# Kernel optimization log

Measured on AMD Instinct MI355X. Metric: run time of the kernel, lower is better.

Reference implementation:

```python
import jax, jax.numpy as jnp
import numpy as np

NUM_RBF = 16
NUM_POS_EMBED = 16
D_MIN, D_MAX = 0.0, 20.0
N_NODES = 20000
N_EDGES = 640000


def _ideal_virtual_cb(bb):
    # bb: [N, 4, 3] with atoms (N, CA, C, O)
    N, CA, C = bb[:, 0], bb[:, 1], bb[:, 2]
    b = CA - N
    c = C - CA
    a = jnp.cross(b, c)
    return -0.58273431 * a + 0.56802827 * b - 0.54067466 * c + CA


def _rbf(D, D_min, D_max, D_count):
    # D: [..., 1] -> [..., D_count]
    D_mu = jnp.linspace(D_min, D_max, D_count, dtype=D.dtype)
    D_sigma = (D_max - D_min) / D_count
    return jnp.exp(-(((D - D_mu) / D_sigma) ** 2))


def _edge_positional_embeddings(edge_index, num_embeddings):
    d = (edge_index[0] - edge_index[1]).astype(jnp.float32)  # [E]
    freq = jnp.exp(
        jnp.arange(0, num_embeddings, 2, dtype=jnp.float32)
        * -(np.log(10000.0) / num_embeddings)
    )  # [num_embeddings//2]
    angles = d[:, None] * freq  # [E, num_embeddings//2]
    return jnp.concatenate([jnp.cos(angles), jnp.sin(angles)], axis=-1)


def setup_inputs() -> dict:
    key = jax.random.key(0)
    k1, k2 = jax.random.split(key)
    bb = jax.random.normal(k1, (N_NODES, 4, 3), dtype=jnp.float32)
    edge_index = jax.random.randint(k2, (2, N_EDGES), 0, N_NODES, dtype=jnp.int64)
    return {"bb": bb, "edge_index": edge_index}


def reference(bb, edge_index, eps=1e-8):
    dst = edge_index[0]
    src = edge_index[1]
    num_edges = edge_index.shape[-1]

    virtual_cb = _ideal_virtual_cb(bb)                     # [N, 3]
    bb5 = jnp.concatenate([bb, virtual_cb[:, None, :]], axis=-2)  # [N, 5, 3]

    edge_bb_src = bb5[src]                                 # [E, 5, 3]
    edge_bb_dst = bb5[dst]                                 # [E, 5, 3]
    diff = edge_bb_src[:, :, None, :] - edge_bb_dst[:, None, :, :] + eps  # [E,5,5,3]
    dists = jnp.linalg.norm(diff, axis=-1)                 # [E, 5, 5]
    dists = dists.reshape(num_edges, -1, 1)                # [E, 25, 1]

    edge_rbf = _rbf(dists, D_MIN, D_MAX, NUM_RBF)          # [E, 25, 16]
    edge_rbf = edge_rbf.reshape(num_edges, -1)             # [E, 400]

    pos = _edge_positional_embeddings(edge_index, NUM_POS_EMBED)  # [E, 16]

    return jnp.concatenate([edge_rbf, pos], axis=-1).astype(jnp.float32)  # [E, 416]
```

## Files before the change

### kernel.cpp

```cpp
#include <hip/hip_runtime.h>
#include <hip/hip_bf16.h>

#define NN 20000
#define NE 640000
#define FEAT 416
#define EPB 16
#define EDGE_BLOCKS (NE / EPB)

typedef float f32x4 __attribute__((ext_vector_type(4)));


__global__ __launch_bounds__(256) void prep_kernel(const float* __restrict__ bb,
                                                   const int* __restrict__ ei,
                                                   int* __restrict__ flag,
                                                   float* __restrict__ bb5) {
    int t = blockIdx.x * 256 + threadIdx.x;

    if (blockIdx.x == 0 && threadIdx.x < 64) {
        int v = ei[2 * threadIdx.x + 1];
        unsigned long long m = __ballot(v != 0);
        if (threadIdx.x == 0) flag[0] = (m == 0ULL) ? 2 : 1;
    }

    if (t < NN) {
        const float* r = bb + (size_t)t * 12;
        float Nx = r[0], Ny = r[1], Nz = r[2];
        float CAx = r[3], CAy = r[4], CAz = r[5];
        float Cx = r[6], Cy = r[7], Cz = r[8];
        float Ox = r[9], Oy = r[10], Oz = r[11];
        float bx = CAx - Nx, by = CAy - Ny, bz = CAz - Nz;
        float cx = Cx - CAx, cy = Cy - CAy, cz = Cz - CAz;
        float ax = by * cz - bz * cy;
        float ay = bz * cx - bx * cz;
        float az = bx * cy - by * cx;
        float vx = -0.58273431f * ax + 0.56802827f * bx - 0.54067466f * cx + CAx;
        float vy = -0.58273431f * ay + 0.56802827f * by - 0.54067466f * cy + CAy;
        float vz = -0.58273431f * az + 0.56802827f * bz - 0.54067466f * cz + CAz;
        float* w = bb5 + (size_t)t * 15;
        w[0] = Nx;  w[1] = Ny;  w[2] = Nz;
        w[3] = CAx; w[4] = CAy; w[5] = CAz;
        w[6] = Cx;  w[7] = Cy;  w[8] = Cz;
        w[9] = Ox;  w[10] = Oy; w[11] = Oz;
        w[12] = vx; w[13] = vy; w[14] = vz;
    }
}

__device__ __forceinline__ void load_idx(const int* __restrict__ ei, int sel, int e,
                                         int& dst, int& src) {
    if (sel == 2) {
        dst = ei[2 * e];
        src = ei[2 * (NE + e)];
    } else {
        dst = ei[e];
        src = ei[NE + e];
    }
}

__global__ __launch_bounds__(256) void edge_kernel(const int* __restrict__ ei,
                                                   const float* __restrict__ bb5,
                                                   const int* __restrict__ flag,
                                                   float* __restrict__ out) {
    __shared__ float dist[EPB * 25];
    __shared__ int sidx[EPB * 2];

    const int tid = threadIdx.x;
    const int e0 = blockIdx.x * EPB;

    if (tid < EPB) {
        int dst, src;
        load_idx(ei, flag[0], e0 + tid, dst, src);
        sidx[tid * 2] = dst;
        sidx[tid * 2 + 1] = src;
    }
    __syncthreads();

    for (int item = tid; item < EPB * 25; item += 256) {
        int s = item / 25;
        int p = item - s * 25;
        int i = p / 5;
        int j = p - i * 5;
        int dst = sidx[s * 2], src = sidx[s * 2 + 1];
        const float* S = bb5 + src * 15 + i * 3;
        const float* D = bb5 + dst * 15 + j * 3;
        float dx = S[0] - D[0] + 1e-8f;
        float dy = S[1] - D[1] + 1e-8f;
        float dz = S[2] - D[2] + 1e-8f;
        dist[item] = sqrtf(dx * dx + dy * dy + dz * dz) * 0.8f;
    }

    f32x4* out4 = reinterpret_cast<f32x4*>(out) + (size_t)e0 * 104;

    if (tid < EPB * 4) {
        int s = tid >> 2;
        int g = tid & 3;
        int dst = sidx[s * 2], src = sidx[s * 2 + 1];
        float d = (float)(dst - src);
        int fb = (g & 1) * 4;
        bool issin = (g >= 2);
        float v[4];
#pragma unroll
        for (int k = 0; k < 4; ++k) {
            int f = fb + k;
            float freq = expf(-(float)f * (float)(9.210340371976184 / 8.0));
            float angle = d * freq;
            double t = (double)angle * 0.15915494309189535;
            double r = t - rint(t);
            float rf = (float)r;
            float val;
            if (issin) {
                asm("v_sin_f32 %0, %1" : "=v"(val) : "v"(rf));
            } else {
                asm("v_cos_f32 %0, %1" : "=v"(val) : "v"(rf));
            }
            v[k] = val;
        }
        f32x4 r4;
        r4.x = v[0]; r4.y = v[1]; r4.z = v[2]; r4.w = v[3];
        __builtin_nontemporal_store(r4, &out4[s * 104 + 100 + g]);
    }
    __syncthreads();

    for (int item = tid; item < EPB * 100; item += 256) {
        int s = item / 100;
        int c = item - s * 100;
        int p = c >> 2;
        int g = c & 3;
        float a = dist[s * 25 + p];
        int k0 = g * 4;
        f32x4 r;
        float u;
        u = a - (float)(k0 + 0) * (16.0f / 15.0f); r.x = __expf(-(u * u));
        u = a - (float)(k0 + 1) * (16.0f / 15.0f); r.y = __expf(-(u * u));
        u = a - (float)(k0 + 2) * (16.0f / 15.0f); r.z = __expf(-(u * u));
        u = a - (float)(k0 + 3) * (16.0f / 15.0f); r.w = __expf(-(u * u));
        __builtin_nontemporal_store(r, &out4[s * 104 + c]);
    }
}

extern "C" void kernel_launch(void* const* d_in, const int* in_sizes, int n_in,
                              void* d_out, int out_size, void* d_ws, size_t ws_size,
                              hipStream_t stream) {
    const float* bb = (const float*)d_in[0];
    const int* ei = (const int*)d_in[1];
    int* flag = (int*)d_ws;
    float* bb5 = (float*)((char*)d_ws + 64);
    float* out = (float*)d_out;

    hipLaunchKernelGGL(prep_kernel, dim3((NN + 255) / 256), dim3(256), 0, stream,
                       bb, ei, flag, bb5);
    hipLaunchKernelGGL(edge_kernel, dim3(EDGE_BLOCKS), dim3(256), 0, stream,
                       ei, bb5, flag, out);
}
```

Before: 228.1 us.

## Fuse virtual-CB prep into edge kernel and drop nontemporal stores

Removes the separate prep kernel and its bb5 workspace. Each edge block now loads the raw backbone rows for its 32 endpoint nodes, computes the virtual CB in registers and stages the 5x3 coordinates in shared memory. Every block redoes the index-format ballot check itself. The aim is to save one launch and the global write and read of bb5, at the cost of recomputing the virtual CB per edge endpoint. Output stores also change from nontemporal to ordinary stores, which alters the cache behaviour for the large output stream.

```diff
diff --git a/kernel.cpp b/kernel.cpp
--- a/kernel.cpp
+++ b/kernel.cpp
@@ -8,42 +8,6 @@
 #define EDGE_BLOCKS (NE / EPB)
 
 typedef float f32x4 __attribute__((ext_vector_type(4)));
-
-
-__global__ __launch_bounds__(256) void prep_kernel(const float* __restrict__ bb,
-                                                   const int* __restrict__ ei,
-                                                   int* __restrict__ flag,
-                                                   float* __restrict__ bb5) {
-    int t = blockIdx.x * 256 + threadIdx.x;
-
-    if (blockIdx.x == 0 && threadIdx.x < 64) {
-        int v = ei[2 * threadIdx.x + 1];
-        unsigned long long m = __ballot(v != 0);
-        if (threadIdx.x == 0) flag[0] = (m == 0ULL) ? 2 : 1;
-    }
-
-    if (t < NN) {
-        const float* r = bb + (size_t)t * 12;
-        float Nx = r[0], Ny = r[1], Nz = r[2];
-        float CAx = r[3], CAy = r[4], CAz = r[5];
-        float Cx = r[6], Cy = r[7], Cz = r[8];
-        float Ox = r[9], Oy = r[10], Oz = r[11];
-        float bx = CAx - Nx, by = CAy - Ny, bz = CAz - Nz;
-        float cx = Cx - CAx, cy = Cy - CAy, cz = Cz - CAz;
-        float ax = by * cz - bz * cy;
-        float ay = bz * cx - bx * cz;
-        float az = bx * cy - by * cx;
-        float vx = -0.58273431f * ax + 0.56802827f * bx - 0.54067466f * cx + CAx;
-        float vy = -0.58273431f * ay + 0.56802827f * by - 0.54067466f * cy + CAy;
-        float vz = -0.58273431f * az + 0.56802827f * bz - 0.54067466f * cz + CAz;
-        float* w = bb5 + (size_t)t * 15;
-        w[0] = Nx;  w[1] = Ny;  w[2] = Nz;
-        w[3] = CAx; w[4] = CAy; w[5] = CAz;
-        w[6] = Cx;  w[7] = Cy;  w[8] = Cz;
-        w[9] = Ox;  w[10] = Oy; w[11] = Oz;
-        w[12] = vx; w[13] = vy; w[14] = vz;
-    }
-}
 
 __device__ __forceinline__ void load_idx(const int* __restrict__ ei, int sel, int e,
                                          int& dst, int& src) {
@@ -56,21 +20,48 @@
     }
 }
 
-__global__ __launch_bounds__(256) void edge_kernel(const int* __restrict__ ei,
-                                                   const float* __restrict__ bb5,
-                                                   const int* __restrict__ flag,
-                                                   float* __restrict__ out) {
+__global__ __launch_bounds__(256) void fused_kernel(const float* __restrict__ bb,
+                                                    const int* __restrict__ ei,
+                                                    float* __restrict__ out) {
+    __shared__ float rows[2 * EPB][17];
     __shared__ float dist[EPB * 25];
     __shared__ int sidx[EPB * 2];
 
     const int tid = threadIdx.x;
     const int e0 = blockIdx.x * EPB;
 
-    if (tid < EPB) {
-        int dst, src;
-        load_idx(ei, flag[0], e0 + tid, dst, src);
-        sidx[tid * 2] = dst;
-        sidx[tid * 2 + 1] = src;
+    if (tid < 64) {
+        int pv = ei[2 * tid + 1];
+        unsigned long long m = __ballot(pv != 0);
+        int sel = (m == 0ULL) ? 2 : 1;
+
+        if (tid < 2 * EPB) {
+            int e = e0 + (tid >> 1);
+            int dst, src;
+            load_idx(ei, sel, e, dst, src);
+            int node = (tid & 1) ? src : dst;
+            sidx[tid] = node;
+            const f32x4* bv = (const f32x4*)bb + (size_t)node * 3;
+            f32x4 v0 = bv[0], v1 = bv[1], v2 = bv[2];
+            float Nx = v0.x, Ny = v0.y, Nz = v0.z;
+            float CAx = v0.w, CAy = v1.x, CAz = v1.y;
+            float Cx = v1.z, Cy = v1.w, Cz = v2.x;
+            float Ox = v2.y, Oy = v2.z, Oz = v2.w;
+            float bx = CAx - Nx, by = CAy - Ny, bz = CAz - Nz;
+            float cx = Cx - CAx, cy = Cy - CAy, cz = Cz - CAz;
+            float ax = by * cz - bz * cy;
+            float ay = bz * cx - bx * cz;
+            float az = bx * cy - by * cx;
+            float vx = -0.58273431f * ax + 0.56802827f * bx - 0.54067466f * cx + CAx;
+            float vy = -0.58273431f * ay + 0.56802827f * by - 0.54067466f * cy + CAy;
+            float vz = -0.58273431f * az + 0.56802827f * bz - 0.54067466f * cz + CAz;
+            float* w = rows[tid];
+            w[0] = Nx;  w[1] = Ny;  w[2] = Nz;
+            w[3] = CAx; w[4] = CAy; w[5] = CAz;
+            w[6] = Cx;  w[7] = Cy;  w[8] = Cz;
+            w[9] = Ox;  w[10] = Oy; w[11] = Oz;
+            w[12] = vx; w[13] = vy; w[14] = vz;
+        }
     }
     __syncthreads();
 
@@ -79,9 +70,8 @@
         int p = item - s * 25;
         int i = p / 5;
         int j = p - i * 5;
-        int dst = sidx[s * 2], src = sidx[s * 2 + 1];
-        const float* S = bb5 + src * 15 + i * 3;
-        const float* D = bb5 + dst * 15 + j * 3;
+        const float* S = rows[2 * s + 1] + i * 3;
+        const float* D = rows[2 * s] + j * 3;
         float dx = S[0] - D[0] + 1e-8f;
         float dy = S[1] - D[1] + 1e-8f;
         float dz = S[2] - D[2] + 1e-8f;
@@ -116,7 +106,7 @@
         }
         f32x4 r4;
         r4.x = v[0]; r4.y = v[1]; r4.z = v[2]; r4.w = v[3];
-        __builtin_nontemporal_store(r4, &out4[s * 104 + 100 + g]);
+        out4[s * 104 + 100 + g] = r4;
     }
     __syncthreads();
 
@@ -133,7 +123,7 @@
         u = a - (float)(k0 + 1) * (16.0f / 15.0f); r.y = __expf(-(u * u));
         u = a - (float)(k0 + 2) * (16.0f / 15.0f); r.z = __expf(-(u * u));
         u = a - (float)(k0 + 3) * (16.0f / 15.0f); r.w = __expf(-(u * u));
-        __builtin_nontemporal_store(r, &out4[s * 104 + c]);
+        out4[s * 104 + c] = r;
     }
 }
 
@@ -142,12 +132,8 @@
                               hipStream_t stream) {
     const float* bb = (const float*)d_in[0];
     const int* ei = (const int*)d_in[1];
-    int* flag = (int*)d_ws;
-    float* bb5 = (float*)((char*)d_ws + 64);
     float* out = (float*)d_out;
 
-    hipLaunchKernelGGL(prep_kernel, dim3((NN + 255) / 256), dim3(256), 0, stream,
-                       bb, ei, flag, bb5);
-    hipLaunchKernelGGL(edge_kernel, dim3(EDGE_BLOCKS), dim3(256), 0, stream,
-                       ei, bb5, flag, out);
+    hipLaunchKernelGGL(fused_kernel, dim3(EDGE_BLOCKS), dim3(256), 0, stream,
+                       bb, ei, out);
 }
```

Result: faster. 213.9 us (-6.2%).
